# Optimization experiments

Hardware: AMD Instinct MI355X
Metric: run time of the kernel (lower is better)

The kernel has to match this reference:

```python
import jax, jax.numpy as jnp
import numpy as np

MARGIN = 0.2

def setup_inputs() -> dict:
    key = jax.random.key(0)
    kx, ky = jax.random.split(key)
    N, D = 8192, 128
    x = jax.random.normal(kx, (N, D), dtype=jnp.float32)
    y = jax.random.normal(ky, (N, D), dtype=jnp.float32)
    return {"x": x, "y": y}

def reference(x, y):
    N = x.shape[0]
    # pairwise squared distances: [N, N]
    xx = jnp.sum(x * x, axis=1)[:, None]
    yy = jnp.sum(y * y, axis=1)[None, :]
    pdist = xx + yy - 2.0 * (x @ y.T)
    d_pos = jnp.diagonal(pdist)  # [N]
    # non-hardest branch: loss = relu(d_pos - pdist + margin), diag zeroed, mean over N*N
    loss = jnp.maximum(d_pos[:, None] - pdist + MARGIN, 0.0)
    off_diag = ~jnp.eye(N, dtype=bool)
    loss = jnp.where(off_diag, loss, 0.0)
    return jnp.mean(loss)
```

## Files before the change

kernel.cpp:

```cpp
#include <hip/hip_runtime.h>
#include <hip/hip_bf16.h>

typedef float f32x4 __attribute__((ext_vector_type(4)));
typedef float f32x2 __attribute__((ext_vector_type(2)));
typedef long  i64;

#define DDIM 128
#define TM 128
#define JCOLS 512
#define MARGIN_F 0.2f

__global__ __launch_bounds__(256)
void prep_v6_kernel(const float* __restrict__ x, const float* __restrict__ y,
                    char* __restrict__ xq, char* __restrict__ yq,
                    float* __restrict__ yy, float* __restrict__ crow)
{
    const int t   = threadIdx.x;
    const int row = blockIdx.x * 16 + (t >> 4);
    const int c   = t & 15;
    const float* xr = x + (size_t)row * DDIM + c * 8;
    const float* yr = y + (size_t)row * DDIM + c * 8;
    const float4 xa = *(const float4*)xr;
    const float4 xc = *(const float4*)(xr + 4);
    const float4 ya = *(const float4*)yr;
    const float4 yc = *(const float4*)(yr + 4);

    int x01 = __builtin_amdgcn_cvt_pk_fp8_f32(2.0f*xa.x, 2.0f*xa.y, 0, false);
    int x23 = __builtin_amdgcn_cvt_pk_fp8_f32(2.0f*xa.z, 2.0f*xa.w, 0, false);
    int x45 = __builtin_amdgcn_cvt_pk_fp8_f32(2.0f*xc.x, 2.0f*xc.y, 0, false);
    int x67 = __builtin_amdgcn_cvt_pk_fp8_f32(2.0f*xc.z, 2.0f*xc.w, 0, false);
    int y01 = __builtin_amdgcn_cvt_pk_fp8_f32(ya.x, ya.y, 0, false);
    int y23 = __builtin_amdgcn_cvt_pk_fp8_f32(ya.z, ya.w, 0, false);
    int y45 = __builtin_amdgcn_cvt_pk_fp8_f32(yc.x, yc.y, 0, false);
    int y67 = __builtin_amdgcn_cvt_pk_fp8_f32(yc.z, yc.w, 0, false);
    int2 xp, yp;
    xp.x = (x01 & 0xffff) | (x23 << 16);  xp.y = (x45 & 0xffff) | (x67 << 16);
    yp.x = (y01 & 0xffff) | (y23 << 16);  yp.y = (y45 & 0xffff) | (y67 << 16);

    const size_t base = (size_t)(row >> 4) * 2048 + (size_t)((c >> 3)) * 1024
                      + (size_t)((c & 3) * 16 + (row & 15)) * 16 + (size_t)(((c >> 2) & 1)) * 8;
    *(int2*)(xq + base) = xp;
    *(int2*)(yq + base) = yp;

    float sy  = ya.x*ya.x + ya.y*ya.y + ya.z*ya.z + ya.w*ya.w
              + yc.x*yc.x + yc.y*yc.y + yc.z*yc.z + yc.w*yc.w;
    float sxy = xa.x*ya.x + xa.y*ya.y + xa.z*ya.z + xa.w*ya.w
              + xc.x*yc.x + xc.y*yc.y + xc.z*yc.z + xc.w*yc.w;
    #pragma unroll
    for (int o = 8; o; o >>= 1) {
        sy  += __shfl_xor(sy,  o);
        sxy += __shfl_xor(sxy, o);
    }
    if (c == 0) {
        yy[row]   = sy;
        crow[row] = sy - 2.0f * sxy + MARGIN_F;
    }
}

__global__ __launch_bounds__(256, 4)
void triplet_v6_kernel(const char* __restrict__ xq, const char* __restrict__ yq,
                       const float* __restrict__ yy, const float* __restrict__ crow,
                       float* __restrict__ partials)
{
    __shared__ float wsum[4];
    const int t    = threadIdx.x;
    const int w    = t >> 6;
    const int lane = t & 63;
    const int l4   = lane >> 4;
    const int l15  = lane & 15;
    const int wm   = w >> 1;
    const int wn   = w & 1;
    const int jg     = blockIdx.x;
    const int istrip = blockIdx.y;

    i64 af[4][4];
    {
        const char* ap = xq + (size_t)(istrip * 8 + wm * 4) * 2048 + (size_t)lane * 16;
        #pragma unroll
        for (int mi = 0; mi < 4; ++mi)
            #pragma unroll
            for (int kk2 = 0; kk2 < 2; ++kk2) {
                const long2 q = *(const long2*)(ap + mi * 2048 + kk2 * 1024);
                af[2*kk2][mi]     = q.x;
                af[2*kk2 + 1][mi] = q.y;
            }
    }
    const int rlo = istrip * TM + wm * 64;
    f32x2 ctv[8];
    #pragma unroll
    for (int mi = 0; mi < 4; ++mi) {
        const float4 c4 = *(const float4*)&crow[rlo + mi * 16 + l4 * 4];
        ctv[mi*2+0] = (f32x2){c4.x, c4.y};
        ctv[mi*2+1] = (f32x2){c4.z, c4.w};
    }

    const int cb0 = jg * 32 + wn * 16;
    f32x2 lsum2[2] = {(f32x2){0.f,0.f}, (f32x2){0.f,0.f}};

    #pragma unroll
    for (int s = 0; s < 16; ++s) {
        const char* bp = yq + (size_t)(cb0 + s) * 2048 + (size_t)lane * 16;
        const long2 q0 = *(const long2*)(bp);
        const long2 q1 = *(const long2*)(bp + 1024);
        i64 bfv[4] = {q0.x, q0.y, q1.x, q1.y};
        const float yyv = yy[(cb0 + s) * 16 + l15];

        f32x4 acc[4] = {};
        #pragma unroll
        for (int kk = 0; kk < 4; ++kk)
            #pragma unroll
            for (int mi = 0; mi < 4; ++mi)
                acc[mi] = __builtin_amdgcn_mfma_f32_16x16x32_fp8_fp8(
                    af[kk][mi], bfv[kk], acc[mi], 0, 0, 0);

        const f32x2 yy2 = (f32x2){yyv, yyv};
        #pragma unroll
        for (int mi = 0; mi < 4; ++mi) {
            #pragma unroll
            for (int rp = 0; rp < 2; ++rp) {
                f32x2 a = (f32x2){acc[mi][2*rp], acc[mi][2*rp+1]};
                a = a + (ctv[mi*2+rp] - yy2);
                lsum2[rp] += __builtin_elementwise_max(a, (f32x2){0.f, 0.f});
            }
        }
    }

    float ls = (lsum2[0][0] + lsum2[0][1]) + (lsum2[1][0] + lsum2[1][1]);
    #pragma unroll
    for (int off = 32; off; off >>= 1) ls += __shfl_xor(ls, off);
    if (lane == 0) wsum[w] = ls;
    __syncthreads();
    if (t == 0)
        partials[blockIdx.y * gridDim.x + blockIdx.x] =
            (wsum[0] + wsum[1]) + (wsum[2] + wsum[3]);
}

__global__ __launch_bounds__(256)
void reduce_v6_kernel(const float* __restrict__ partials, float* __restrict__ out,
                      float inv_n2, float diag_corr)
{
    __shared__ float wsum[4];
    const int t = threadIdx.x;
    float s = partials[t] + partials[t + 256] + partials[t + 512] + partials[t + 768];
    #pragma unroll
    for (int off = 32; off; off >>= 1) s += __shfl_xor(s, off);
    if ((t & 63) == 0) wsum[t >> 6] = s;
    __syncthreads();
    if (t == 0)
        out[0] = ((wsum[0] + wsum[1]) + (wsum[2] + wsum[3])) * inv_n2 + diag_corr;
}


#define TILE 128
#define LDSK 136
typedef __bf16 bf16x8 __attribute__((ext_vector_type(8)));

__global__ __launch_bounds__(256)
void prep_f32_kernel(const float* __restrict__ x, const float* __restrict__ y,
                     float* __restrict__ yy, float* __restrict__ crow,
                     float* __restrict__ out)
{
    const int t    = threadIdx.x;
    const int lane = t & 63;
    const int row  = blockIdx.x * 4 + (t >> 6);
    const float2 xv = ((const float2*)(x + (size_t)row * DDIM))[lane];
    const float2 yv = ((const float2*)(y + (size_t)row * DDIM))[lane];
    float sy  = yv.x * yv.x + yv.y * yv.y;
    float sxy = xv.x * yv.x + xv.y * yv.y;
    #pragma unroll
    for (int off = 32; off; off >>= 1) {
        sy  += __shfl_xor(sy,  off);
        sxy += __shfl_xor(sxy, off);
    }
    if (lane == 0) { yy[row] = sy; crow[row] = sy - 2.0f * sxy; }
    if (t == 0 && blockIdx.x == 0) out[0] = 0.0f;
}

__global__ __launch_bounds__(256)
void triplet_f32_kernel(const float* __restrict__ x, const float* __restrict__ y,
                        const float* __restrict__ yy, const float* __restrict__ crow,
                        float* __restrict__ out, float inv_n2)
{
    __shared__ __bf16 As[TILE][LDSK];
    __shared__ __bf16 Bs[TILE][LDSK];
    __shared__ float ctile[TILE];
    __shared__ float yytile[TILE];
    __shared__ float wsum[4];

    const int t  = threadIdx.x;
    const int bi = blockIdx.y;
    const int bj = blockIdx.x;
    {
        const int rr = t >> 4;
        const int cc = (t & 15) * 8;
        const float* xp = x + (size_t)bi * TILE * DDIM;
        const float* yp = y + (size_t)bj * TILE * DDIM;
        #pragma unroll
        for (int it = 0; it < 8; ++it) {
            const int r = it * 16 + rr;
            const float4 a0 = *(const float4*)(xp + (size_t)r * DDIM + cc);
            const float4 a1 = *(const float4*)(xp + (size_t)r * DDIM + cc + 4);
            bf16x8 av;
            av[0] = (__bf16)a0.x; av[1] = (__bf16)a0.y; av[2] = (__bf16)a0.z; av[3] = (__bf16)a0.w;
            av[4] = (__bf16)a1.x; av[5] = (__bf16)a1.y; av[6] = (__bf16)a1.z; av[7] = (__bf16)a1.w;
            *(bf16x8*)&As[r][cc] = av;
            const float4 b0 = *(const float4*)(yp + (size_t)r * DDIM + cc);
            const float4 b1 = *(const float4*)(yp + (size_t)r * DDIM + cc + 4);
            bf16x8 bv;
            bv[0] = (__bf16)b0.x; bv[1] = (__bf16)b0.y; bv[2] = (__bf16)b0.z; bv[3] = (__bf16)b0.w;
            bv[4] = (__bf16)b1.x; bv[5] = (__bf16)b1.y; bv[6] = (__bf16)b1.z; bv[7] = (__bf16)b1.w;
            *(bf16x8*)&Bs[r][cc] = bv;
        }
        if (t < TILE) ctile[t]         = crow[bi * TILE + t];
        else          yytile[t - TILE] = yy[bj * TILE + (t - TILE)];
    }
    __syncthreads();

    const int wave = t >> 6;
    const int lane = t & 63;
    const int wm   = wave >> 1;
    const int wn   = wave & 1;
    const int l4   = lane >> 4;
    const int l15  = lane & 15;

    f32x4 acc[4][4] = {};
    #pragma unroll
    for (int kk = 0; kk < 4; ++kk) {
        const int kb = kk * 32 + l4 * 8;
        bf16x8 af[4], bfv[4];
        #pragma unroll
        for (int mi = 0; mi < 4; ++mi) af[mi] = *(const bf16x8*)&As[wm * 64 + mi * 16 + l15][kb];
        #pragma unroll
        for (int ni = 0; ni < 4; ++ni) bfv[ni] = *(const bf16x8*)&Bs[wn * 64 + ni * 16 + l15][kb];
        #pragma unroll
        for (int mi = 0; mi < 4; ++mi)
            #pragma unroll
            for (int ni = 0; ni < 4; ++ni)
                acc[mi][ni] = __builtin_amdgcn_mfma_f32_16x16x32_bf16(af[mi], bfv[ni], acc[mi][ni], 0, 0, 0);
    }

    float lsum = 0.0f;
    #pragma unroll
    for (int ni = 0; ni < 4; ++ni) {
        const int ct    = wn * 64 + ni * 16 + l15;
        const float yyv = yytile[ct];
        const int gj    = bj * TILE + ct;
        #pragma unroll
        for (int mi = 0; mi < 4; ++mi)
            #pragma unroll
            for (int r = 0; r < 4; ++r) {
                const int rt = wm * 64 + mi * 16 + l4 * 4 + r;
                float v = fmaxf(2.0f * acc[mi][ni][r] + ctile[rt] - yyv + MARGIN_F, 0.0f);
                if (bi * TILE + rt == gj) v = 0.0f;
                lsum += v;
            }
    }
    #pragma unroll
    for (int off = 32; off; off >>= 1) lsum += __shfl_xor(lsum, off);
    if (lane == 0) wsum[wave] = lsum;
    __syncthreads();
    if (t == 0) atomicAdd(out, (wsum[0] + wsum[1] + wsum[2] + wsum[3]) * inv_n2);
}


extern "C" void kernel_launch(void* const* d_in, const int* in_sizes, int n_in,
                              void* d_out, int out_size, void* d_ws, size_t ws_size,
                              hipStream_t stream)
{
    const float* x = (const float*)d_in[0];
    const float* y = (const float*)d_in[1];
    float* out = (float*)d_out;
    const int N = in_sizes[0] / DDIM;
    const float inv_n2 = 1.0f / ((float)N * (float)N);

    const size_t q_bytes = (size_t)N * DDIM;
    const size_t need = 2 * q_bytes + 2 * (size_t)N * sizeof(float) + 4096 * sizeof(float);

    if (ws_size >= need && (N % JCOLS) == 0) {
        char*  xq  = (char*)d_ws;
        char*  yq  = xq + q_bytes;
        float* yy  = (float*)(yq + q_bytes);
        float* crw = yy + N;
        float* par = crw + N;
        const float diag_corr = -MARGIN_F / (float)N;
        prep_v6_kernel<<<dim3(N / 16), dim3(256), 0, stream>>>(x, y, xq, yq, yy, crw);
        triplet_v6_kernel<<<dim3(N / JCOLS, N / TM), dim3(256), 0, stream>>>(
            xq, yq, yy, crw, par);
        reduce_v6_kernel<<<dim3(1), dim3(256), 0, stream>>>(par, out, inv_n2, diag_corr);
    } else {
        float* yy  = (float*)d_ws;
        float* crw = yy + N;
        prep_f32_kernel<<<dim3(N / 4), dim3(256), 0, stream>>>(x, y, yy, crw, out);
        triplet_f32_kernel<<<dim3(N / TILE, N / TILE), dim3(256), 0, stream>>>(
            x, y, yy, crw, out, inv_n2);
    }
}
```

Before: 76.89 us.

## Switch to 16x16x128 scaled FP8 MFMA with matching fragment layout

Replaces four 16x16x32 FP8 MFMAs per tile with a single gfx950 16x16x128 scaled MFMA (unit scales), and changes the prep kernel's quantized layout so each lane loads 32 contiguous bytes per fragment. It also hoists the yy loads out of the inner loop into a register array. The goal is to cut MFMA issue count and load instructions; the costs are higher register pressure and reliance on the new instruction's operand layout matching the packing.

```diff
diff --git a/kernel.cpp b/kernel.cpp
--- a/kernel.cpp
+++ b/kernel.cpp
@@ -3,7 +3,7 @@
 
 typedef float f32x4 __attribute__((ext_vector_type(4)));
 typedef float f32x2 __attribute__((ext_vector_type(2)));
-typedef long  i64;
+typedef int   i32x8 __attribute__((ext_vector_type(8)));
 
 #define DDIM 128
 #define TM 128
@@ -11,7 +11,7 @@
 #define MARGIN_F 0.2f
 
 __global__ __launch_bounds__(256)
-void prep_v6_kernel(const float* __restrict__ x, const float* __restrict__ y,
+void prep_v7_kernel(const float* __restrict__ x, const float* __restrict__ y,
                     char* __restrict__ xq, char* __restrict__ yq,
                     float* __restrict__ yy, float* __restrict__ crow)
 {
@@ -37,8 +37,8 @@
     xp.x = (x01 & 0xffff) | (x23 << 16);  xp.y = (x45 & 0xffff) | (x67 << 16);
     yp.x = (y01 & 0xffff) | (y23 << 16);  yp.y = (y45 & 0xffff) | (y67 << 16);
 
-    const size_t base = (size_t)(row >> 4) * 2048 + (size_t)((c >> 3)) * 1024
-                      + (size_t)((c & 3) * 16 + (row & 15)) * 16 + (size_t)(((c >> 2) & 1)) * 8;
+    const size_t base = (size_t)(row >> 4) * 2048
+                      + (size_t)((c >> 2) * 16 + (row & 15)) * 32 + (size_t)(c & 3) * 8;
     *(int2*)(xq + base) = xp;
     *(int2*)(yq + base) = yp;
 
@@ -58,7 +58,7 @@
 }
 
 __global__ __launch_bounds__(256, 4)
-void triplet_v6_kernel(const char* __restrict__ xq, const char* __restrict__ yq,
+void triplet_v7_kernel(const char* __restrict__ xq, const char* __restrict__ yq,
                        const float* __restrict__ yy, const float* __restrict__ crow,
                        float* __restrict__ partials)
 {
@@ -73,17 +73,15 @@
     const int jg     = blockIdx.x;
     const int istrip = blockIdx.y;
 
-    i64 af[4][4];
+    i32x8 af[4];
     {
-        const char* ap = xq + (size_t)(istrip * 8 + wm * 4) * 2048 + (size_t)lane * 16;
-        #pragma unroll
-        for (int mi = 0; mi < 4; ++mi)
-            #pragma unroll
-            for (int kk2 = 0; kk2 < 2; ++kk2) {
-                const long2 q = *(const long2*)(ap + mi * 2048 + kk2 * 1024);
-                af[2*kk2][mi]     = q.x;
-                af[2*kk2 + 1][mi] = q.y;
-            }
+        const char* ap = xq + (size_t)(istrip * 8 + wm * 4) * 2048 + (size_t)lane * 32;
+        #pragma unroll
+        for (int mi = 0; mi < 4; ++mi) {
+            const int4 p0 = *(const int4*)(ap + mi * 2048);
+            const int4 p1 = *(const int4*)(ap + mi * 2048 + 16);
+            af[mi] = (i32x8){p0.x, p0.y, p0.z, p0.w, p1.x, p1.y, p1.z, p1.w};
+        }
     }
     const int rlo = istrip * TM + wm * 64;
     f32x2 ctv[8];
@@ -93,27 +91,29 @@
         ctv[mi*2+0] = (f32x2){c4.x, c4.y};
         ctv[mi*2+1] = (f32x2){c4.z, c4.w};
     }
-
     const int cb0 = jg * 32 + wn * 16;
+    float yyv[16];
+    #pragma unroll
+    for (int s = 0; s < 16; ++s)
+        yyv[s] = yy[(cb0 + s) * 16 + l15];
+
     f32x2 lsum2[2] = {(f32x2){0.f,0.f}, (f32x2){0.f,0.f}};
 
     #pragma unroll
     for (int s = 0; s < 16; ++s) {
-        const char* bp = yq + (size_t)(cb0 + s) * 2048 + (size_t)lane * 16;
-        const long2 q0 = *(const long2*)(bp);
-        const long2 q1 = *(const long2*)(bp + 1024);
-        i64 bfv[4] = {q0.x, q0.y, q1.x, q1.y};
-        const float yyv = yy[(cb0 + s) * 16 + l15];
+        const char* bp = yq + (size_t)(cb0 + s) * 2048 + (size_t)lane * 32;
+        const int4 q0 = *(const int4*)(bp);
+        const int4 q1 = *(const int4*)(bp + 16);
+        const i32x8 bfv = (i32x8){q0.x, q0.y, q0.z, q0.w, q1.x, q1.y, q1.z, q1.w};
 
         f32x4 acc[4] = {};
         #pragma unroll
-        for (int kk = 0; kk < 4; ++kk)
-            #pragma unroll
-            for (int mi = 0; mi < 4; ++mi)
-                acc[mi] = __builtin_amdgcn_mfma_f32_16x16x32_fp8_fp8(
-                    af[kk][mi], bfv[kk], acc[mi], 0, 0, 0);
-
-        const f32x2 yy2 = (f32x2){yyv, yyv};
+        for (int mi = 0; mi < 4; ++mi)
+            acc[mi] = __builtin_amdgcn_mfma_scale_f32_16x16x128_f8f6f4(
+                af[mi], bfv, acc[mi], 0, 0,
+                0, 127, 0, 127);
+
+        const f32x2 yy2 = (f32x2){yyv[s], yyv[s]};
         #pragma unroll
         for (int mi = 0; mi < 4; ++mi) {
             #pragma unroll
@@ -136,7 +136,7 @@
 }
 
 __global__ __launch_bounds__(256)
-void reduce_v6_kernel(const float* __restrict__ partials, float* __restrict__ out,
+void reduce_v7_kernel(const float* __restrict__ partials, float* __restrict__ out,
                       float inv_n2, float diag_corr)
 {
     __shared__ float wsum[4];
@@ -283,10 +283,10 @@
         float* crw = yy + N;
         float* par = crw + N;
         const float diag_corr = -MARGIN_F / (float)N;
-        prep_v6_kernel<<<dim3(N / 16), dim3(256), 0, stream>>>(x, y, xq, yq, yy, crw);
-        triplet_v6_kernel<<<dim3(N / JCOLS, N / TM), dim3(256), 0, stream>>>(
+        prep_v7_kernel<<<dim3(N / 16), dim3(256), 0, stream>>>(x, y, xq, yq, yy, crw);
+        triplet_v7_kernel<<<dim3(N / JCOLS, N / TM), dim3(256), 0, stream>>>(
             xq, yq, yy, crw, par);
-        reduce_v6_kernel<<<dim3(1), dim3(256), 0, stream>>>(par, out, inv_n2, diag_corr);
+        reduce_v7_kernel<<<dim3(1), dim3(256), 0, stream>>>(par, out, inv_n2, diag_corr);
     } else {
         float* yy  = (float*)d_ws;
         float* crw = yy + N;
```

New measurement: 71.67 us (median of 2 runs). 6.8% less time.
